# Kernel optimization log

Hardware: AMD Instinct MI355X
Metric: run time of the kernel (lower is better)

The kernel has to match this reference:

```python
import jax, jax.numpy as jnp
import numpy as np

VOXEL = 128
N_PTS = VOXEL ** 3  # 2,097,152
C_FEAT = 14
T_HASH = 4194304


def _hash_index(coords, table_size):
    # Instant-NGP style spatial hash: elementwise prime multiply, xor-reduce, mod T.
    # uint32 arithmetic emulates the wrap-around semantics of the integer hash.
    primes = jnp.array([1, 2654435761, 805459861], dtype=jnp.uint32)
    h = coords.astype(jnp.uint32) * primes  # [N, 3]
    return ((h[:, 0] ^ h[:, 1]) ^ h[:, 2]) % jnp.uint32(table_size)  # [N]


def _quat_to_rotmat(q):
    # q: [N, 4] normalized, (r, x, y, z) convention (standard 3DGS)
    r, x, y, z = q[:, 0], q[:, 1], q[:, 2], q[:, 3]
    R = jnp.stack([
        1 - 2 * (y * y + z * z), 2 * (x * y - r * z), 2 * (x * z + r * y),
        2 * (x * y + r * z), 1 - 2 * (x * x + z * z), 2 * (y * z - r * x),
        2 * (x * z - r * y), 2 * (y * z + r * x), 1 - 2 * (x * x + y * y),
    ], axis=-1)
    return R.reshape(-1, 3, 3)


def setup_inputs() -> dict:
    key = jax.random.key(0)
    k1, k2, k3 = jax.random.split(key, 3)
    coordinates = jax.random.randint(k1, (N_PTS, 3), 0, VOXEL, dtype=jnp.int32)
    hash_table = jax.random.normal(k2, (C_FEAT, T_HASH), dtype=jnp.float32)
    camera_center = jax.random.normal(k3, (3,), dtype=jnp.float32)
    far = jnp.ones((1,), dtype=jnp.float32)
    return {"coordinates": coordinates, "hash_table": hash_table,
            "camera_center": camera_center, "far": far, "voxel_size": VOXEL}


def reference(coordinates, hash_table, camera_center, far, voxel_size):
    far_s = far[0]
    vs = jnp.float32(voxel_size)

    # hash_query: [C, N] gather from hash table
    idx = _hash_index(coordinates, hash_table.shape[1])
    gf = hash_table[:, idx]  # [14, N]

    # compute_voxel_center: [N, 3]
    voxel_center = (coordinates.astype(jnp.float32) / vs * 2 * far_s
                    - far_s + camera_center[None, :] + far_s / vs)

    # delta means: normalize over ALL elements (torch.mean/std on full tensor, unbiased std)
    dm = gf[0:3].T  # [N, 3]
    dm = (dm - jnp.mean(dm)) / jnp.std(dm, ddof=1) * 2 * far_s / vs / 6.0
    means = dm + voxel_center  # [N, 3]

    # covariance from scaling + rotation (standard 3DGS)
    scales = jax.nn.sigmoid(gf[7:10].T) * 2 * far_s / vs  # [N, 3]
    q = gf[3:7].T
    q = q / jnp.linalg.norm(q, axis=-1, keepdims=True)
    R = _quat_to_rotmat(q)                       # [N, 3, 3]
    L = R * scales[:, None, :]                   # L = R @ diag(s)
    covariances = jnp.einsum('nij,nkj->nik', L, L)  # [N, 3, 3]

    harmonics = gf[10:13].T[:, :, None]          # [N, 3, 1] (raw features)
    opacities = jax.nn.sigmoid(gf[13] - 4.0)     # [N]

    n = coordinates.shape[0]
    return (means[None], covariances[None], harmonics[None], opacities[None])
```

## Files before the change

kernel.cpp:

```cpp
#include <hip/hip_runtime.h>
#include <math.h>

#define N_PTS (128*128*128)
#define T_HASH 4194304
#define T_MASK (T_HASH - 1)
#define ENTRY_STRIDE 16

__device__ __forceinline__ unsigned hash_idx(int x, int y, int z) {
    return ((unsigned)x ^ ((unsigned)y * 2654435761u)
                        ^ ((unsigned)z * 805459861u)) & T_MASK;
}

__global__ void transpose_kernel(const float* __restrict__ table,
                                 float* __restrict__ tt) {
    __shared__ float sh[256 * 17];
    const int t  = threadIdx.x;
    const int i0 = blockIdx.x * 256;

    #pragma unroll
    for (int j = 0; j < 14; ++j)
        sh[t * 17 + j] = table[(size_t)j * T_HASH + i0 + t];
    sh[t * 17 + 14] = 0.f;
    sh[t * 17 + 15] = 0.f;
    __syncthreads();

    float4* dst = (float4*)(tt + (size_t)i0 * ENTRY_STRIDE);
    #pragma unroll
    for (int k = 0; k < 4; ++k) {
        const int f = t + k * 256;
        const int p = f >> 2;
        const int c = f & 3;
        const float* s = &sh[p * 17 + c * 4];
        dst[f] = make_float4(s[0], s[1], s[2], s[3]);
    }
}

__global__ void reduce_kernel_t(const int* __restrict__ coords,
                                const float* __restrict__ tt,
                                double* __restrict__ acc) {
    float s = 0.f, ss = 0.f;
    const int stride = gridDim.x * blockDim.x;
    for (int i = blockIdx.x * blockDim.x + threadIdx.x; i < N_PTS; i += stride) {
        const unsigned idx = hash_idx(coords[i*3], coords[i*3+1], coords[i*3+2]);
        const float4 f = *(const float4*)(tt + (size_t)idx * ENTRY_STRIDE);
        s  += f.x + f.y + f.z;
        ss += f.x * f.x + f.y * f.y + f.z * f.z;
    }
    #pragma unroll
    for (int off = 32; off > 0; off >>= 1) {
        s  += __shfl_down(s, off, 64);
        ss += __shfl_down(ss, off, 64);
    }
    __shared__ float sh_s[4], sh_ss[4];
    const int lane = threadIdx.x & 63;
    const int wid  = threadIdx.x >> 6;
    if (lane == 0) { sh_s[wid] = s; sh_ss[wid] = ss; }
    __syncthreads();
    if (threadIdx.x == 0) {
        float ts = 0.f, tss = 0.f;
        for (int w = 0; w < 4; ++w) { ts += sh_s[w]; tss += sh_ss[w]; }
        atomicAdd(&acc[0], (double)ts);
        atomicAdd(&acc[1], (double)tss);
    }
}

__global__ void reduce_kernel_o(const int* __restrict__ coords,
                                const float* __restrict__ table,
                                double* __restrict__ acc) {
    float s = 0.f, ss = 0.f;
    const int stride = gridDim.x * blockDim.x;
    for (int i = blockIdx.x * blockDim.x + threadIdx.x; i < N_PTS; i += stride) {
        const unsigned idx = hash_idx(coords[i*3], coords[i*3+1], coords[i*3+2]);
        float g0 = table[idx];
        float g1 = table[T_HASH + idx];
        float g2 = table[2 * T_HASH + idx];
        s  += g0 + g1 + g2;
        ss += g0 * g0 + g1 * g1 + g2 * g2;
    }
    #pragma unroll
    for (int off = 32; off > 0; off >>= 1) {
        s  += __shfl_down(s, off, 64);
        ss += __shfl_down(ss, off, 64);
    }
    __shared__ float sh_s[4], sh_ss[4];
    const int lane = threadIdx.x & 63;
    const int wid  = threadIdx.x >> 6;
    if (lane == 0) { sh_s[wid] = s; sh_ss[wid] = ss; }
    __syncthreads();
    if (threadIdx.x == 0) {
        float ts = 0.f, tss = 0.f;
        for (int w = 0; w < 4; ++w) { ts += sh_s[w]; tss += sh_ss[w]; }
        atomicAdd(&acc[0], (double)ts);
        atomicAdd(&acc[1], (double)tss);
    }
}

template <bool TRANSPOSED>
__global__ void main_kernel(const int* __restrict__ coords,
                            const float* __restrict__ tab,
                            const float* __restrict__ cam,
                            const float* __restrict__ far_p,
                            const int* __restrict__ vs_p,
                            const double* __restrict__ acc,
                            float* __restrict__ out) {
    const int i = blockIdx.x * blockDim.x + threadIdx.x;
    if (i >= N_PTS) return;

    const float far_s = far_p[0];
    const float vs    = (float)vs_p[0];

    const double n      = 3.0 * (double)N_PTS;
    const double sum    = acc[0];
    const double sumsq  = acc[1];
    const double mean_d = sum / n;
    const double var_d  = (sumsq - sum * sum / n) / (n - 1.0);
    const float mean    = (float)mean_d;
    const float inv_std = (float)(1.0 / sqrt(var_d));

    const int cx = coords[i * 3 + 0];
    const int cy = coords[i * 3 + 1];
    const int cz = coords[i * 3 + 2];
    const unsigned idx = hash_idx(cx, cy, cz);

    float g[16];
    if (TRANSPOSED) {
        const float4* e = (const float4*)(tab + (size_t)idx * ENTRY_STRIDE);
        float4 f0 = e[0], f1 = e[1], f2 = e[2], f3 = e[3];
        g[0]=f0.x; g[1]=f0.y; g[2]=f0.z; g[3]=f0.w;
        g[4]=f1.x; g[5]=f1.y; g[6]=f1.z; g[7]=f1.w;
        g[8]=f2.x; g[9]=f2.y; g[10]=f2.z; g[11]=f2.w;
        g[12]=f3.x; g[13]=f3.y;
    } else {
        #pragma unroll
        for (int j = 0; j < 14; ++j)
            g[j] = tab[(size_t)j * T_HASH + idx];
    }

    const float two_far_over_vs = 2.f * far_s / vs;
    const float dm_scale = two_far_over_vs / 6.f;
    const float c_f[3] = { (float)cx, (float)cy, (float)cz };
    #pragma unroll
    for (int k = 0; k < 3; ++k) {
        const float vc = c_f[k] / vs * 2.f * far_s - far_s + cam[k] + far_s / vs;
        out[(size_t)i * 3 + k] = (g[k] - mean) * inv_std * dm_scale + vc;
    }

    float qr = g[3], qx = g[4], qy = g[5], qz = g[6];
    const float qinv = 1.f / sqrtf(qr * qr + qx * qx + qy * qy + qz * qz);
    qr *= qinv; qx *= qinv; qy *= qinv; qz *= qinv;

    float R[3][3];
    R[0][0] = 1.f - 2.f * (qy * qy + qz * qz);
    R[0][1] = 2.f * (qx * qy - qr * qz);
    R[0][2] = 2.f * (qx * qz + qr * qy);
    R[1][0] = 2.f * (qx * qy + qr * qz);
    R[1][1] = 1.f - 2.f * (qx * qx + qz * qz);
    R[1][2] = 2.f * (qy * qz - qr * qx);
    R[2][0] = 2.f * (qx * qz - qr * qy);
    R[2][1] = 2.f * (qy * qz + qr * qx);
    R[2][2] = 1.f - 2.f * (qx * qx + qy * qy);

    float sc[3];
    #pragma unroll
    for (int k = 0; k < 3; ++k)
        sc[k] = two_far_over_vs / (1.f + expf(-g[7 + k]));

    float* covp = out + (size_t)3 * N_PTS + (size_t)i * 9;
    #pragma unroll
    for (int r = 0; r < 3; ++r) {
        #pragma unroll
        for (int c = 0; c < 3; ++c) {
            float a = 0.f;
            #pragma unroll
            for (int j = 0; j < 3; ++j)
                a += (R[r][j] * sc[j]) * (R[c][j] * sc[j]);
            covp[r * 3 + c] = a;
        }
    }

    float* harp = out + (size_t)12 * N_PTS + (size_t)i * 3;
    #pragma unroll
    for (int k = 0; k < 3; ++k)
        harp[k] = g[10 + k];

    out[(size_t)15 * N_PTS + i] = 1.f / (1.f + expf(-(g[13] - 4.f)));
}

extern "C" void kernel_launch(void* const* d_in, const int* in_sizes, int n_in,
                              void* d_out, int out_size, void* d_ws, size_t ws_size,
                              hipStream_t stream) {
    const int*   coords = (const int*)d_in[0];
    const float* table  = (const float*)d_in[1];
    const float* cam    = (const float*)d_in[2];
    const float* far_p  = (const float*)d_in[3];
    const int*   vs_p   = (const int*)d_in[4];
    float*       out    = (float*)d_out;

    double* acc = (double*)d_ws;
    float*  tt  = (float*)((char*)d_ws + 256);

    const size_t need = 256 + (size_t)T_HASH * ENTRY_STRIDE * sizeof(float);

    hipMemsetAsync(d_ws, 0, 2 * sizeof(double), stream);

    const int threads = 256;
    const int blocks  = (N_PTS + threads - 1) / threads;

    if (ws_size >= need) {
        transpose_kernel<<<T_HASH / 256, 256, 0, stream>>>(table, tt);
        reduce_kernel_t<<<2048, 256, 0, stream>>>(coords, tt, acc);
        main_kernel<true><<<blocks, threads, 0, stream>>>(coords, tt, cam, far_p,
                                                          vs_p, acc, out);
    } else {
        reduce_kernel_o<<<2048, 256, 0, stream>>>(coords, table, acc);
        main_kernel<false><<<blocks, threads, 0, stream>>>(coords, table, cam,
                                                           far_p, vs_p, acc, out);
    }
}
```

Measured before the change: 542.6 us.

## Fuse reduction into main gather pass and finalize means in separate pass

Merges the mean/std reduction pass with the main per-point compute, so the hash-table gather happens once instead of twice. Means are written raw and a small finalize kernel applies normalization after the global statistics are known. The transpose kernel now uses float4 coalesced loads over 512 entries per block and processes four points per thread with batched loads for more memory-level parallelism. In exchange, the means are written and read back once more, and the coordinates are reloaded.

```diff
diff --git a/kernel.cpp b/kernel.cpp
--- a/kernel.cpp
+++ b/kernel.cpp
@@ -6,46 +6,134 @@
 #define T_MASK (T_HASH - 1)
 #define ENTRY_STRIDE 16
 
+#define PA_BLOCKS  2048
+#define PA_THREADS 256
+#define PA_STRIDE  (PA_BLOCKS * PA_THREADS)
+#define PA_ITERS   (N_PTS / PA_STRIDE)
+
 __device__ __forceinline__ unsigned hash_idx(int x, int y, int z) {
     return ((unsigned)x ^ ((unsigned)y * 2654435761u)
                         ^ ((unsigned)z * 805459861u)) & T_MASK;
 }
 
-__global__ void transpose_kernel(const float* __restrict__ table,
-                                 float* __restrict__ tt) {
-    __shared__ float sh[256 * 17];
+__global__ __launch_bounds__(256)
+void transpose_kernel(const float* __restrict__ table, float* __restrict__ tt) {
+    __shared__ float sh[16][516];
     const int t  = threadIdx.x;
-    const int i0 = blockIdx.x * 256;
-
-    #pragma unroll
-    for (int j = 0; j < 14; ++j)
-        sh[t * 17 + j] = table[(size_t)j * T_HASH + i0 + t];
-    sh[t * 17 + 14] = 0.f;
-    sh[t * 17 + 15] = 0.f;
+    const int i0 = blockIdx.x * 512;
+
+    const int col4  = (t & 127) * 4;
+    const int rhalf = t >> 7;
+    #pragma unroll
+    for (int k = 0; k < 7; ++k) {
+        const int row = 2 * k + rhalf;
+        const float4 v = *(const float4*)(table + (size_t)row * T_HASH + i0 + col4);
+        *(float4*)&sh[row][col4] = v;
+    }
     __syncthreads();
 
+    const int c  = t & 3;
+    const int r0 = c * 4;
+    const int p0 = t >> 2;
     float4* dst = (float4*)(tt + (size_t)i0 * ENTRY_STRIDE);
     #pragma unroll
-    for (int k = 0; k < 4; ++k) {
-        const int f = t + k * 256;
-        const int p = f >> 2;
-        const int c = f & 3;
-        const float* s = &sh[p * 17 + c * 4];
-        dst[f] = make_float4(s[0], s[1], s[2], s[3]);
-    }
-}
-
-__global__ void reduce_kernel_t(const int* __restrict__ coords,
-                                const float* __restrict__ tt,
-                                double* __restrict__ acc) {
+    for (int k = 0; k < 8; ++k) {
+        const int p = p0 + k * 64;
+        float vx = sh[r0 + 0][p];
+        float vy = sh[r0 + 1][p];
+        float vz = sh[r0 + 2][p];
+        float vw = sh[r0 + 3][p];
+        if (c == 3) { vz = 0.f; vw = 0.f; }
+        dst[(size_t)p * 4 + c] = make_float4(vx, vy, vz, vw);
+    }
+}
+
+__global__ __launch_bounds__(256)
+void fused_main_kernel(const int*   __restrict__ coords,
+                       const float* __restrict__ tt,
+                       const float* __restrict__ far_p,
+                       const int*   __restrict__ vs_p,
+                       float*       __restrict__ out,
+                       double*      __restrict__ acc) {
+    const int base = blockIdx.x * PA_THREADS + threadIdx.x;
+
+    int cx[PA_ITERS], cy[PA_ITERS], cz[PA_ITERS];
+    #pragma unroll
+    for (int it = 0; it < PA_ITERS; ++it) {
+        const size_t b = (size_t)(base + it * PA_STRIDE) * 3;
+        cx[it] = coords[b + 0];
+        cy[it] = coords[b + 1];
+        cz[it] = coords[b + 2];
+    }
+
+    float4 f0[PA_ITERS], f1[PA_ITERS], f2[PA_ITERS], f3[PA_ITERS];
+    #pragma unroll
+    for (int it = 0; it < PA_ITERS; ++it) {
+        const unsigned idx = hash_idx(cx[it], cy[it], cz[it]);
+        const float4* e = (const float4*)(tt + (size_t)idx * ENTRY_STRIDE);
+        f0[it] = e[0]; f1[it] = e[1]; f2[it] = e[2]; f3[it] = e[3];
+    }
+
+    const float far_s = far_p[0];
+    const float vs    = (float)vs_p[0];
+    const float tfv   = 2.f * far_s / vs;
+
     float s = 0.f, ss = 0.f;
-    const int stride = gridDim.x * blockDim.x;
-    for (int i = blockIdx.x * blockDim.x + threadIdx.x; i < N_PTS; i += stride) {
-        const unsigned idx = hash_idx(coords[i*3], coords[i*3+1], coords[i*3+2]);
-        const float4 f = *(const float4*)(tt + (size_t)idx * ENTRY_STRIDE);
-        s  += f.x + f.y + f.z;
-        ss += f.x * f.x + f.y * f.y + f.z * f.z;
-    }
+    #pragma unroll
+    for (int it = 0; it < PA_ITERS; ++it) {
+        const int i = base + it * PA_STRIDE;
+
+        const float g0 = f0[it].x, g1 = f0[it].y, g2 = f0[it].z;
+        out[(size_t)i * 3 + 0] = g0;
+        out[(size_t)i * 3 + 1] = g1;
+        out[(size_t)i * 3 + 2] = g2;
+        s  += g0 + g1 + g2;
+        ss += g0 * g0 + g1 * g1 + g2 * g2;
+
+        float qr = f0[it].w, qx = f1[it].x, qy = f1[it].y, qz = f1[it].z;
+        const float qinv = 1.f / sqrtf(qr * qr + qx * qx + qy * qy + qz * qz);
+        qr *= qinv; qx *= qinv; qy *= qinv; qz *= qinv;
+
+        float R[3][3];
+        R[0][0] = 1.f - 2.f * (qy * qy + qz * qz);
+        R[0][1] = 2.f * (qx * qy - qr * qz);
+        R[0][2] = 2.f * (qx * qz + qr * qy);
+        R[1][0] = 2.f * (qx * qy + qr * qz);
+        R[1][1] = 1.f - 2.f * (qx * qx + qz * qz);
+        R[1][2] = 2.f * (qy * qz - qr * qx);
+        R[2][0] = 2.f * (qx * qz - qr * qy);
+        R[2][1] = 2.f * (qy * qz + qr * qx);
+        R[2][2] = 1.f - 2.f * (qx * qx + qy * qy);
+
+        float sc[3];
+        sc[0] = tfv / (1.f + expf(-f1[it].w));
+        sc[1] = tfv / (1.f + expf(-f2[it].x));
+        sc[2] = tfv / (1.f + expf(-f2[it].y));
+
+        float L[3][3];
+        #pragma unroll
+        for (int r = 0; r < 3; ++r)
+            #pragma unroll
+            for (int j = 0; j < 3; ++j)
+                L[r][j] = R[r][j] * sc[j];
+
+        float* covp = out + (size_t)3 * N_PTS + (size_t)i * 9;
+        #pragma unroll
+        for (int r = 0; r < 3; ++r)
+            #pragma unroll
+            for (int col = 0; col < 3; ++col)
+                covp[r * 3 + col] = L[r][0] * L[col][0]
+                                  + L[r][1] * L[col][1]
+                                  + L[r][2] * L[col][2];
+
+        float* harp = out + (size_t)12 * N_PTS + (size_t)i * 3;
+        harp[0] = f2[it].z;
+        harp[1] = f2[it].w;
+        harp[2] = f3[it].x;
+
+        out[(size_t)15 * N_PTS + i] = 1.f / (1.f + expf(-(f3[it].y - 4.f)));
+    }
+
     #pragma unroll
     for (int off = 32; off > 0; off >>= 1) {
         s  += __shfl_down(s, off, 64);
@@ -61,6 +149,40 @@
         for (int w = 0; w < 4; ++w) { ts += sh_s[w]; tss += sh_ss[w]; }
         atomicAdd(&acc[0], (double)ts);
         atomicAdd(&acc[1], (double)tss);
+    }
+}
+
+__global__ __launch_bounds__(256)
+void finalize_means_kernel(const int*    __restrict__ coords,
+                           const float*  __restrict__ cam,
+                           const float*  __restrict__ far_p,
+                           const int*    __restrict__ vs_p,
+                           const double* __restrict__ acc,
+                           float*        __restrict__ out) {
+    const double n      = 3.0 * (double)N_PTS;
+    const double sum    = acc[0];
+    const double sumsq  = acc[1];
+    const float  mean   = (float)(sum / n);
+    const float  inv_std= (float)(1.0 / sqrt((sumsq - sum * sum / n) / (n - 1.0)));
+
+    const float far_s = far_p[0];
+    const float vs    = (float)vs_p[0];
+    const float a     = inv_std * (2.f * far_s / vs / 6.f);
+    const float off_c = -far_s + far_s / vs;
+    const float cam_t[3] = { cam[0], cam[1], cam[2] };
+
+    const int base = blockIdx.x * PA_THREADS + threadIdx.x;
+    #pragma unroll
+    for (int it = 0; it < PA_ITERS; ++it) {
+        const int i = base + it * PA_STRIDE;
+        const size_t b = (size_t)i * 3;
+        const int cc[3] = { coords[b + 0], coords[b + 1], coords[b + 2] };
+        #pragma unroll
+        for (int k = 0; k < 3; ++k) {
+            const float vc = (float)cc[k] / vs * 2.f * far_s + off_c + cam_t[k];
+            const float dm = out[b + k];
+            out[b + k] = (dm - mean) * a + vc;
+        }
     }
 }
 
@@ -95,14 +217,13 @@
     }
 }
 
-template <bool TRANSPOSED>
-__global__ void main_kernel(const int* __restrict__ coords,
-                            const float* __restrict__ tab,
-                            const float* __restrict__ cam,
-                            const float* __restrict__ far_p,
-                            const int* __restrict__ vs_p,
-                            const double* __restrict__ acc,
-                            float* __restrict__ out) {
+__global__ void main_kernel_o(const int* __restrict__ coords,
+                              const float* __restrict__ tab,
+                              const float* __restrict__ cam,
+                              const float* __restrict__ far_p,
+                              const int* __restrict__ vs_p,
+                              const double* __restrict__ acc,
+                              float* __restrict__ out) {
     const int i = blockIdx.x * blockDim.x + threadIdx.x;
     if (i >= N_PTS) return;
 
@@ -112,29 +233,18 @@
     const double n      = 3.0 * (double)N_PTS;
     const double sum    = acc[0];
     const double sumsq  = acc[1];
-    const double mean_d = sum / n;
-    const double var_d  = (sumsq - sum * sum / n) / (n - 1.0);
-    const float mean    = (float)mean_d;
-    const float inv_std = (float)(1.0 / sqrt(var_d));
+    const float mean    = (float)(sum / n);
+    const float inv_std = (float)(1.0 / sqrt((sumsq - sum * sum / n) / (n - 1.0)));
 
     const int cx = coords[i * 3 + 0];
     const int cy = coords[i * 3 + 1];
     const int cz = coords[i * 3 + 2];
     const unsigned idx = hash_idx(cx, cy, cz);
 
-    float g[16];
-    if (TRANSPOSED) {
-        const float4* e = (const float4*)(tab + (size_t)idx * ENTRY_STRIDE);
-        float4 f0 = e[0], f1 = e[1], f2 = e[2], f3 = e[3];
-        g[0]=f0.x; g[1]=f0.y; g[2]=f0.z; g[3]=f0.w;
-        g[4]=f1.x; g[5]=f1.y; g[6]=f1.z; g[7]=f1.w;
-        g[8]=f2.x; g[9]=f2.y; g[10]=f2.z; g[11]=f2.w;
-        g[12]=f3.x; g[13]=f3.y;
-    } else {
-        #pragma unroll
-        for (int j = 0; j < 14; ++j)
-            g[j] = tab[(size_t)j * T_HASH + idx];
-    }
+    float g[14];
+    #pragma unroll
+    for (int j = 0; j < 14; ++j)
+        g[j] = tab[(size_t)j * T_HASH + idx];
 
     const float two_far_over_vs = 2.f * far_s / vs;
     const float dm_scale = two_far_over_vs / 6.f;
@@ -203,17 +313,18 @@
 
     hipMemsetAsync(d_ws, 0, 2 * sizeof(double), stream);
 
-    const int threads = 256;
-    const int blocks  = (N_PTS + threads - 1) / threads;
-
     if (ws_size >= need) {
-        transpose_kernel<<<T_HASH / 256, 256, 0, stream>>>(table, tt);
-        reduce_kernel_t<<<2048, 256, 0, stream>>>(coords, tt, acc);
-        main_kernel<true><<<blocks, threads, 0, stream>>>(coords, tt, cam, far_p,
-                                                          vs_p, acc, out);
+        transpose_kernel<<<T_HASH / 512, 256, 0, stream>>>(table, tt);
+        fused_main_kernel<<<PA_BLOCKS, PA_THREADS, 0, stream>>>(coords, tt, far_p,
+                                                                vs_p, out, acc);
+        finalize_means_kernel<<<PA_BLOCKS, PA_THREADS, 0, stream>>>(coords, cam,
+                                                                    far_p, vs_p,
+                                                                    acc, out);
     } else {
+        const int threads = 256;
+        const int blocks  = (N_PTS + threads - 1) / threads;
         reduce_kernel_o<<<2048, 256, 0, stream>>>(coords, table, acc);
-        main_kernel<false><<<blocks, threads, 0, stream>>>(coords, table, cam,
-                                                           far_p, vs_p, acc, out);
-    }
-}
+        main_kernel_o<<<blocks, threads, 0, stream>>>(coords, table, cam,
+                                                      far_p, vs_p, acc, out);
+    }
+}
```

Result: faster. 511.2 us (-5.8%).
